# Performance work log

Hardware: AMD Instinct MI355X
Metric: run time of the kernel (lower is better)

The kernel has to match this reference:

```python
import jax, jax.numpy as jnp
import numpy as np

B, S, E, D, A, V, EM, T = 128, 196, 2048, 512, 256, 10000, 512, 20


def setup_inputs() -> dict:
    key = jax.random.key(0)
    ks = jax.random.split(key, 16)
    def rn(k, shape, scale=0.02):
        return jax.random.normal(k, shape, dtype=jnp.float32) * scale
    return {
        "encoder_features": jax.random.normal(ks[0], (B, S, E), dtype=jnp.float32),
        "captions": jax.random.randint(ks[1], (B, T), 0, V),
        "emb_table": rn(ks[2], (V, EM)),
        "W_ea": rn(ks[3], (E, A)), "b_ea": jnp.zeros((A,), jnp.float32),
        "W_da": rn(ks[4], (D, A)), "b_da": jnp.zeros((A,), jnp.float32),
        "W_fa": rn(ks[5], (A, 1)), "b_fa": jnp.zeros((1,), jnp.float32),
        "W_ih": rn(ks[6], (EM + E, 4 * D)), "b_ih": jnp.zeros((4 * D,), jnp.float32),
        "W_hh": rn(ks[7], (D, 4 * D)), "b_hh": jnp.zeros((4 * D,), jnp.float32),
        "W_cp": rn(ks[8], (E, EM)), "b_cp": jnp.zeros((EM,), jnp.float32),
        "W_hp": rn(ks[9], (D, EM)), "b_hp": jnp.zeros((EM,), jnp.float32),
        "W_op": rn(ks[10], (EM, V)), "b_op": jnp.zeros((V,), jnp.float32),
        "W_inith": rn(ks[11], (E, D)), "b_inith": jnp.zeros((D,), jnp.float32),
        "W_initc": rn(ks[12], (E, D)), "b_initc": jnp.zeros((D,), jnp.float32),
    }


def reference(encoder_features, captions, emb_table, W_ea, b_ea, W_da, b_da,
              W_fa, b_fa, W_ih, b_ih, W_hh, b_hh, W_cp, b_cp, W_hp, b_hp,
              W_op, b_op, W_inith, b_inith, W_initc, b_initc):
    # init LSTM state from mean-pooled encoder features
    mean_feat = encoder_features.mean(axis=1)            # [B, E]
    h0 = mean_feat @ W_inith + b_inith                   # [B, D]
    c0 = mean_feat @ W_initc + b_initc                   # [B, D]
    # encoder branch of Bahdanau attention is step-invariant: precompute
    enc_att = jnp.einsum('bse,ea->bsa', encoder_features, W_ea) + b_ea  # [B, S, A]
    embs = emb_table[captions]                           # [B, T, EM]
    xs = jnp.swapaxes(embs, 0, 1)                        # [T, B, EM]

    def step(carry, x_t):
        h, c = carry
        # Bahdanau: relu(enc_att + dec_att) -> score -> softmax -> context
        dec_att = h @ W_da + b_da                        # [B, A]
        combined = jax.nn.relu(enc_att + dec_att[:, None, :])  # [B, S, A]
        scores = (combined @ W_fa)[..., 0] + b_fa[0]     # [B, S]
        alpha = jax.nn.softmax(scores, axis=1)           # [B, S]
        context = jnp.einsum('bs,bse->be', alpha, encoder_features)  # [B, E]
        # LSTMCell on [embedding; context]
        x_in = jnp.concatenate([x_t, context], axis=-1)  # [B, EM+E]
        gates = x_in @ W_ih + b_ih + h @ W_hh + b_hh     # [B, 4D]
        i, f, g, o = jnp.split(gates, 4, axis=-1)
        c_new = jax.nn.sigmoid(f) * c + jax.nn.sigmoid(i) * jnp.tanh(g)
        h_new = jax.nn.sigmoid(o) * jnp.tanh(c_new)
        # output: proj(context) + proj(hidden) -> vocab logits (dropout = eval identity)
        feat = context @ W_cp + b_cp + h_new @ W_hp + b_hp  # [B, EM]
        logits = feat @ W_op + b_op                      # [B, V]
        return (h_new, c_new), logits

    _, logits = jax.lax.scan(step, (h0, c0), xs)         # [T, B, V]
    return jnp.swapaxes(logits, 0, 1)                    # [B, T, V]
```

## Files before the change

### kernel.cpp

```cpp
#include <hip/hip_runtime.h>
#include <hip/hip_bf16.h>

#define B 128
#define S 196
#define E 2048
#define D 512
#define A 256
#define V 10000
#define EM 512
#define T 20
#define KCAT 2560

typedef unsigned short u16;
typedef __bf16 bf16x8 __attribute__((ext_vector_type(8)));
typedef float f32x4 __attribute__((ext_vector_type(4)));
typedef u16 u16x8 __attribute__((ext_vector_type(8)));
typedef u16 u16x4 __attribute__((ext_vector_type(4)));

__device__ inline u16 f2bf(float f) {
    union { float f; unsigned u; } x; x.f = f;
    return (u16)((x.u + 0x7FFFu + ((x.u >> 16) & 1u)) >> 16);
}
__device__ inline float bf2f(u16 h) {
    union { unsigned u; float f; } x; x.u = ((unsigned)h) << 16;
    return x.f;
}
__device__ inline bf16x8 ld_bf8(const u16* p) {
    return __builtin_bit_cast(bf16x8, *reinterpret_cast<const u16x8*>(p));
}
__device__ inline bf16x8 cvt_bf8(const float* p) {
    float4 u = *reinterpret_cast<const float4*>(p);
    float4 v = *reinterpret_cast<const float4*>(p + 4);
    u16x8 t;
    t[0] = f2bf(u.x); t[1] = f2bf(u.y); t[2] = f2bf(u.z); t[3] = f2bf(u.w);
    t[4] = f2bf(v.x); t[5] = f2bf(v.y); t[6] = f2bf(v.z); t[7] = f2bf(v.w);
    return __builtin_bit_cast(bf16x8, t);
}
__device__ inline float sigm(float x) { return 1.f / (1.f + expf(-x)); }

struct PairT {
    const void* Ap;
    long lda;
    const u16* Bt;
    long ldb;
    int K;
};

template <int NP, bool AF32, typename OutT, int WTM, int WTN, int WVM, int WVN>
__global__ __launch_bounds__(WVM * WVN * 64) void gemm_mfma(
    int N, PairT q0, PairT q1, PairT q2,
    const float* __restrict__ bias1, const float* __restrict__ bias2,
    OutT* __restrict__ Cc, long ldc)
{
    const int tid  = threadIdx.x;
    const int w    = tid >> 6;
    const int lane = tid & 63;
    const int lr   = lane & 15;
    const int lg   = lane >> 4;
    const int mrow = blockIdx.y * (WVM * WTM * 16) + (w / WVN) * (WTM * 16);
    const int ncol = blockIdx.x * (WVN * WTN * 16) + (w % WVN) * (WTN * 16);

    f32x4 acc[WTM][WTN];
#pragma unroll
    for (int i = 0; i < WTM; ++i)
#pragma unroll
        for (int j = 0; j < WTN; ++j) acc[i][j] = (f32x4){0.f, 0.f, 0.f, 0.f};

    const PairT qs[3] = {q0, q1, q2};
#pragma unroll
    for (int p = 0; p < NP; ++p) {
        const PairT pp = qs[p];
        const int nk = pp.K >> 5;
        const u16*   Ab = (const u16*)pp.Ap;
        const float* Af = (const float*)pp.Ap;
        size_t aoff[WTM];
#pragma unroll
        for (int mi = 0; mi < WTM; ++mi)
            aoff[mi] = (size_t)(mrow + mi * 16 + lr) * pp.lda + lg * 8;
        const u16* Bp = pp.Bt + (size_t)(ncol + lr) * pp.ldb + lg * 8;

#pragma unroll 2
        for (int kk = 0; kk < nk; ++kk) {
            const int ko = kk * 32;
            bf16x8 av[WTM], bv[WTN];
#pragma unroll
            for (int mi = 0; mi < WTM; ++mi) {
                if (AF32) av[mi] = cvt_bf8(Af + aoff[mi] + ko);
                else      av[mi] = ld_bf8(Ab + aoff[mi] + ko);
            }
#pragma unroll
            for (int ni = 0; ni < WTN; ++ni)
                bv[ni] = ld_bf8(Bp + ko + (size_t)(ni * 16) * pp.ldb);
#pragma unroll
            for (int mi = 0; mi < WTM; ++mi)
#pragma unroll
                for (int ni = 0; ni < WTN; ++ni)
                    acc[mi][ni] = __builtin_amdgcn_mfma_f32_16x16x32_bf16(
                        av[mi], bv[ni], acc[mi][ni], 0, 0, 0);
        }
    }

#pragma unroll
    for (int ni = 0; ni < WTN; ++ni) {
        const int col = ncol + ni * 16 + lr;
        if (col >= N) continue;
        float bs = 0.f;
        if (bias1) bs += bias1[col];
        if (bias2) bs += bias2[col];
#pragma unroll
        for (int mi = 0; mi < WTM; ++mi) {
#pragma unroll
            for (int r = 0; r < 4; ++r) {
                const int row = mrow + mi * 16 + lg * 4 + r;
                const float v = acc[mi][ni][r] + bs;
                if constexpr (sizeof(OutT) == 2)
                    Cc[(size_t)row * ldc + col] = (OutT)f2bf(v);
                else
                    Cc[(size_t)row * ldc + col] = v;
            }
        }
    }
}

__global__ __launch_bounds__(256) void gemm_enc(
    const u16* __restrict__ Abf,
    const u16* __restrict__ Bt,
    const float* __restrict__ bias,
    u16* __restrict__ Cc)
{
    __shared__ u16 As[128 * 64];
    __shared__ u16 Bs[128 * 64];

    const int tid  = threadIdx.x;
    const int w    = tid >> 6;
    const int lane = tid & 63;
    const int lr   = lane & 15;
    const int lg   = lane >> 4;
    const int brow = blockIdx.y * 128;
    const int bcol = blockIdx.x * 128;
    const int wrow = (w >> 1) * 64;
    const int wcol = (w & 1) * 64;

    int arow[4], acb[4], aphys[4];
#pragma unroll
    for (int i = 0; i < 4; ++i) {
        const int s = (tid + 256 * i) * 16;
        arow[i]  = s >> 7;
        acb[i]   = s & 127;
        aphys[i] = (s ^ ((arow[i] & 7) << 4)) >> 1;
    }

    int aoff[2][4], boff[2][4];
#pragma unroll
    for (int kh = 0; kh < 2; ++kh) {
#pragma unroll
        for (int i = 0; i < 4; ++i) {
            const int ra = wrow + i * 16 + lr;
            aoff[kh][i] = (((ra << 7) + (kh << 6) + (lg << 4)) ^ ((ra & 7) << 4)) >> 1;
            const int rb = wcol + i * 16 + lr;
            boff[kh][i] = (((rb << 7) + (kh << 6) + (lg << 4)) ^ ((rb & 7) << 4)) >> 1;
        }
    }

    f32x4 acc[4][4];
#pragma unroll
    for (int i = 0; i < 4; ++i)
#pragma unroll
        for (int j = 0; j < 4; ++j) acc[i][j] = (f32x4){0.f, 0.f, 0.f, 0.f};

    for (int k0 = 0; k0 < 2048; k0 += 64) {
        u16x8 av[4], bv[4];
#pragma unroll
        for (int i = 0; i < 4; ++i) {
            av[i] = *reinterpret_cast<const u16x8*>(
                Abf + (size_t)(brow + arow[i]) * 2048 + k0 + (acb[i] >> 1));
            bv[i] = *reinterpret_cast<const u16x8*>(
                Bt + (size_t)(bcol + arow[i]) * 2048 + k0 + (acb[i] >> 1));
        }
        __syncthreads();
#pragma unroll
        for (int i = 0; i < 4; ++i) {
            *reinterpret_cast<u16x8*>(As + aphys[i]) = av[i];
            *reinterpret_cast<u16x8*>(Bs + aphys[i]) = bv[i];
        }
        __syncthreads();

#pragma unroll
        for (int kh = 0; kh < 2; ++kh) {
            bf16x8 af[4], bf_[4];
#pragma unroll
            for (int mi = 0; mi < 4; ++mi)
                af[mi] = __builtin_bit_cast(bf16x8,
                    *reinterpret_cast<const u16x8*>(As + aoff[kh][mi]));
#pragma unroll
            for (int ni = 0; ni < 4; ++ni)
                bf_[ni] = __builtin_bit_cast(bf16x8,
                    *reinterpret_cast<const u16x8*>(Bs + boff[kh][ni]));
#pragma unroll
            for (int mi = 0; mi < 4; ++mi)
#pragma unroll
                for (int ni = 0; ni < 4; ++ni)
                    acc[mi][ni] = __builtin_amdgcn_mfma_f32_16x16x32_bf16(
                        af[mi], bf_[ni], acc[mi][ni], 0, 0, 0);
        }
    }

#pragma unroll
    for (int ni = 0; ni < 4; ++ni) {
        const int col = bcol + wcol + ni * 16 + lr;
        const float bs = bias[col];
#pragma unroll
        for (int mi = 0; mi < 4; ++mi) {
#pragma unroll
            for (int r = 0; r < 4; ++r) {
                const int row = brow + wrow + mi * 16 + lg * 4 + r;
                Cc[(size_t)row * 256 + col] = f2bf(acc[mi][ni][r] + bs);
            }
        }
    }
}

__global__ __launch_bounds__(256) void init_xin_h(
    const u16* __restrict__ h_cur, u16* __restrict__ xin)
{
    const int idx = blockIdx.x * 256 + threadIdx.x;
    const int b = idx >> 9;
    const int d = idx & (D - 1);
    xin[(size_t)b * KCAT + 2048 + d] = h_cur[idx];
}

template <bool FBF>
__global__ __launch_bounds__(256) void alpha_ctx_lstm(
    const void* __restrict__ Fv,
    const u16*  __restrict__ enc,
    const u16*  __restrict__ W_daT,
    const float* __restrict__ b_da,
    const float* __restrict__ W_fa,
    const float* __restrict__ b_ih_,
    const float* __restrict__ b_hh_,
    const float* __restrict__ egates,
    const float* __restrict__ part,
    const float* __restrict__ c_rd,
    float* __restrict__ c_wr,
    const u16*  __restrict__ h0,
    u16* __restrict__ h_all,
    u16* __restrict__ ctx_all,
    u16* __restrict__ xin,
    int t)
{
    const int blk  = blockIdx.x;
    const int tid  = threadIdx.x;
    const int w    = tid >> 6;
    const int lane = tid & 63;
    const int b    = blk >> 1;
    const int q    = blk & 1;

    __shared__ float hl[D];
    __shared__ float dec[A];
    __shared__ float wfa[A];
    __shared__ float sc[S];
    __shared__ float red[8];

    if (t == 0) {
        hl[tid]       = bf2f(h0[b * D + tid]);
        hl[tid + 256] = bf2f(h0[b * D + 256 + tid]);
    } else {
        const int tt = t - 1;
#pragma unroll
        for (int half = 0; half < 2; ++half) {
            const int d = tid + half * 256;
            float g4[4];
#pragma unroll
            for (int g = 0; g < 4; ++g) {
                const int col = ((d >> 4) << 6) + (g << 4) + (d & 15);
                float s = b_ih_[g * D + d] + b_hh_[g * D + d] +
                          egates[((size_t)(b * T + tt) << 11) + col];
#pragma unroll
                for (int z = 0; z < 8; ++z)
                    s += part[((size_t)(z * B + b) << 11) + col];
                g4[g] = s;
            }
            const int idx = (b << 9) + d;
            const float cn = sigm(g4[1]) * c_rd[idx] + sigm(g4[0]) * tanhf(g4[2]);
            const float hf = sigm(g4[3]) * tanhf(cn);
            hl[d] = hf;
            if (q == 0) {
                c_wr[idx] = cn;
                const u16 hv = f2bf(hf);
                h_all[((size_t)(b * T + tt)) * D + d] = hv;
                xin[(size_t)b * KCAT + 2048 + d] = hv;
            }
        }
    }
    wfa[tid] = W_fa[tid];
    __syncthreads();

    {
        float acc = 0.f;
        const u16* wr = W_daT + (size_t)tid * D;
#pragma unroll 4
        for (int i = 0; i < D / 8; ++i) {
            const u16x8 v = *reinterpret_cast<const u16x8*>(wr + i * 8);
#pragma unroll
            for (int j = 0; j < 8; ++j) acc += bf2f(v[j]) * hl[i * 8 + j];
        }
        dec[tid] = acc + b_da[tid];
    }
    __syncthreads();

    if (tid < S) {
        const u16* er = enc + ((size_t)b * S + tid) * A;
        float v = 0.f;
#pragma unroll 4
        for (int i = 0; i < A / 8; ++i) {
            const u16x8 e8 = *reinterpret_cast<const u16x8*>(er + i * 8);
#pragma unroll
            for (int j = 0; j < 8; ++j) {
                float x = bf2f(e8[j]) + dec[i * 8 + j];
                x = x > 0.f ? x : 0.f;
                v += x * wfa[i * 8 + j];
            }
        }
        sc[tid] = v;
    }
    __syncthreads();

    float m = -1e30f;
    for (int s = tid; s < S; s += 256) m = fmaxf(m, sc[s]);
    for (int off = 32; off; off >>= 1) m = fmaxf(m, __shfl_down(m, off));
    if (lane == 0) red[w] = m;
    __syncthreads();
    if (tid == 0) red[0] = fmaxf(fmaxf(red[0], red[1]), fmaxf(red[2], red[3]));
    __syncthreads();
    m = red[0];

    float sum = 0.f;
    for (int s = tid; s < S; s += 256) {
        const float ev = __expf(sc[s] - m);
        sc[s] = ev;
        sum += ev;
    }
    for (int off = 32; off; off >>= 1) sum += __shfl_down(sum, off);
    if (lane == 0) red[4 + w] = sum;
    __syncthreads();
    if (tid == 0) red[4] = red[4] + red[5] + red[6] + red[7];
    __syncthreads();
    const float inv = 1.f / red[4];

    {
        const int e0 = q * 1024 + tid * 4;
        float a0 = 0.f, a1 = 0.f, a2 = 0.f, a3 = 0.f;
        float b0 = 0.f, b1 = 0.f, b2 = 0.f, b3 = 0.f;
        float c0 = 0.f, c1 = 0.f, c2 = 0.f, c3 = 0.f;
        float d0 = 0.f, d1 = 0.f, d2 = 0.f, d3 = 0.f;
        if (FBF) {
            const u16* F0 = (const u16*)Fv + (size_t)b * S * E + e0;
            const u16* F1 = F0 + (size_t)49 * E;
            const u16* F2 = F0 + (size_t)98 * E;
            const u16* F3 = F0 + (size_t)147 * E;
#pragma unroll 7
            for (int s = 0; s < 49; ++s) {
                const u16x4 v0 = *reinterpret_cast<const u16x4*>(F0 + (size_t)s * E);
                const u16x4 v1 = *reinterpret_cast<const u16x4*>(F1 + (size_t)s * E);
                const u16x4 v2 = *reinterpret_cast<const u16x4*>(F2 + (size_t)s * E);
                const u16x4 v3 = *reinterpret_cast<const u16x4*>(F3 + (size_t)s * E);
                const float l0 = sc[s], l1 = sc[s + 49], l2 = sc[s + 98], l3 = sc[s + 147];
                a0 += l0 * bf2f(v0[0]); a1 += l0 * bf2f(v0[1]);
                a2 += l0 * bf2f(v0[2]); a3 += l0 * bf2f(v0[3]);
                b0 += l1 * bf2f(v1[0]); b1 += l1 * bf2f(v1[1]);
                b2 += l1 * bf2f(v1[2]); b3 += l1 * bf2f(v1[3]);
                c0 += l2 * bf2f(v2[0]); c1 += l2 * bf2f(v2[1]);
                c2 += l2 * bf2f(v2[2]); c3 += l2 * bf2f(v2[3]);
                d0 += l3 * bf2f(v3[0]); d1 += l3 * bf2f(v3[1]);
                d2 += l3 * bf2f(v3[2]); d3 += l3 * bf2f(v3[3]);
            }
        } else {
            const float* F0 = (const float*)Fv + (size_t)b * S * E + e0;
            const float* F1 = F0 + (size_t)49 * E;
            const float* F2 = F0 + (size_t)98 * E;
            const float* F3 = F0 + (size_t)147 * E;
#pragma unroll 7
            for (int s = 0; s < 49; ++s) {
                const float4 v0 = *reinterpret_cast<const float4*>(F0 + (size_t)s * E);
                const float4 v1 = *reinterpret_cast<const float4*>(F1 + (size_t)s * E);
                const float4 v2 = *reinterpret_cast<const float4*>(F2 + (size_t)s * E);
                const float4 v3 = *reinterpret_cast<const float4*>(F3 + (size_t)s * E);
                const float l0 = sc[s], l1 = sc[s + 49], l2 = sc[s + 98], l3 = sc[s + 147];
                a0 += l0 * v0.x; a1 += l0 * v0.y; a2 += l0 * v0.z; a3 += l0 * v0.w;
                b0 += l1 * v1.x; b1 += l1 * v1.y; b2 += l1 * v1.z; b3 += l1 * v1.w;
                c0 += l2 * v2.x; c1 += l2 * v2.y; c2 += l2 * v2.z; c3 += l2 * v2.w;
                d0 += l3 * v3.x; d1 += l3 * v3.y; d2 += l3 * v3.z; d3 += l3 * v3.w;
            }
        }
        a0 += b0 + c0 + d0; a1 += b1 + c1 + d1;
        a2 += b2 + c2 + d2; a3 += b3 + c3 + d3;
        u16x4 o;
        o[0] = f2bf(a0 * inv); o[1] = f2bf(a1 * inv);
        o[2] = f2bf(a2 * inv); o[3] = f2bf(a3 * inv);
        *reinterpret_cast<u16x4*>(ctx_all + ((size_t)(b * T + t)) * E + e0) = o;
        *reinterpret_cast<u16x4*>(xin + (size_t)b * KCAT + e0) = o;
    }
}

__global__ __launch_bounds__(128) void gates_split8(
    const u16* __restrict__ xin, const u16* __restrict__ W_chT,
    float* __restrict__ part)
{
    const int tid  = threadIdx.x;
    const int w    = tid >> 6;
    const int lane = tid & 63;
    const int lr   = lane & 15;
    const int lg   = lane >> 4;
    const int mrow = blockIdx.y * 16;
    const int ncol = blockIdx.x * 128 + w * 64;
    const int z    = blockIdx.z;
    const int kb   = z * 320;

    f32x4 acc[4];
#pragma unroll
    for (int j = 0; j < 4; ++j) acc[j] = (f32x4){0.f, 0.f, 0.f, 0.f};

    const u16* Ap = xin + (size_t)(mrow + lr) * KCAT + kb + lg * 8;
    const u16* Bp = W_chT + (size_t)(ncol + lr) * KCAT + kb + lg * 8;

#pragma unroll
    for (int kk = 0; kk < 10; ++kk) {
        const int ko = kk * 32;
        const bf16x8 av = ld_bf8(Ap + ko);
        bf16x8 bv[4];
#pragma unroll
        for (int ni = 0; ni < 4; ++ni)
            bv[ni] = ld_bf8(Bp + ko + (size_t)(ni * 16) * KCAT);
#pragma unroll
        for (int ni = 0; ni < 4; ++ni)
            acc[ni] = __builtin_amdgcn_mfma_f32_16x16x32_bf16(av, bv[ni], acc[ni], 0, 0, 0);
    }

#pragma unroll
    for (int ni = 0; ni < 4; ++ni) {
        const int col = ncol + ni * 16 + lr;
#pragma unroll
        for (int r = 0; r < 4; ++r) {
            const int row = mrow + lg * 4 + r;
            part[((size_t)(z * B + row) << 11) + col] = acc[ni][r];
        }
    }
}

__global__ __launch_bounds__(256) void lstm_last(
    const float* __restrict__ part,
    const float* __restrict__ egates,
    const float* __restrict__ b_ih_, const float* __restrict__ b_hh_,
    const float* __restrict__ c_rd,
    u16* __restrict__ h_all)
{
    const int idx = blockIdx.x * 256 + threadIdx.x;
    const int b = idx >> 9;
    const int d = idx & (D - 1);
    const int tt = T - 1;
    float g4[4];
#pragma unroll
    for (int g = 0; g < 4; ++g) {
        const int col = ((d >> 4) << 6) + (g << 4) + (d & 15);
        float s = b_ih_[g * D + d] + b_hh_[g * D + d] +
                  egates[((size_t)(b * T + tt) << 11) + col];
#pragma unroll
        for (int z = 0; z < 8; ++z)
            s += part[((size_t)(z * B + b) << 11) + col];
        g4[g] = s;
    }
    const float cn = sigm(g4[1]) * c_rd[idx] + sigm(g4[0]) * tanhf(g4[2]);
    h_all[((size_t)(b * T + tt)) * D + d] = f2bf(sigm(g4[3]) * tanhf(cn));
}

__global__ __launch_bounds__(256) void transpose_bf(
    const float* __restrict__ in, int K, int N, u16* __restrict__ out)
{
    __shared__ float tls[32][33];
    const int k0 = blockIdx.y * 32, n0 = blockIdx.x * 32;
    const int c = threadIdx.x & 31, r8 = threadIdx.x >> 5;
#pragma unroll
    for (int i = 0; i < 4; ++i) {
        const int k = r8 + i * 8;
        float v = 0.f;
        if (n0 + c < N) v = in[(size_t)(k0 + k) * N + n0 + c];
        tls[k][c] = v;
    }
    __syncthreads();
#pragma unroll
    for (int i = 0; i < 4; ++i) {
        const int n = r8 + i * 8;
        out[(size_t)(n0 + n) * K + k0 + c] = f2bf(tls[c][n]);
    }
}

__global__ __launch_bounds__(256) void transpose_bf_gates(
    const float* __restrict__ in, int Kin, u16* __restrict__ out, int ldo, int ko)
{
    __shared__ float tls[32][33];
    const int k0 = blockIdx.y * 32, n0 = blockIdx.x * 32;
    const int c = threadIdx.x & 31, r8 = threadIdx.x >> 5;
#pragma unroll
    for (int i = 0; i < 4; ++i) {
        const int k = r8 + i * 8;
        tls[k][c] = in[(size_t)(k0 + k) * 2048 + n0 + c];
    }
    __syncthreads();
#pragma unroll
    for (int i = 0; i < 4; ++i) {
        const int nn = r8 + i * 8;
        const int n = n0 + nn;
        const int g = n >> 9, d = n & (D - 1);
        const int orow = ((d >> 4) << 6) + (g << 4) + (d & 15);
        out[(size_t)orow * ldo + ko + k0 + c] = f2bf(tls[c][nn]);
    }
}

template <bool WRITE>
__global__ __launch_bounds__(256) void conv_mean(
    const float* __restrict__ F, u16* __restrict__ Fbf, u16* __restrict__ meanbf)
{
    const int idx = blockIdx.x * 256 + threadIdx.x;
    const int b = idx >> 11;
    const int e = idx & (E - 1);
    const float* src = F + (size_t)b * S * E + e;
    float acc = 0.f;
#pragma unroll 2
    for (int s = 0; s < S; ++s) {
        const float v = src[(size_t)s * E];
        acc += v;
        if (WRITE) Fbf[(size_t)b * S * E + (size_t)s * E + e] = f2bf(v);
    }
    meanbf[idx] = f2bf(acc * (1.f / (float)S));
}

__global__ __launch_bounds__(256) void gather_embs_bf(
    const int* __restrict__ captions, const float* __restrict__ table,
    u16* __restrict__ out)
{
    const int idx = blockIdx.x * 256 + threadIdx.x;
    const int row = idx >> 6;
    const int ch  = idx & 63;
    const int cap = captions[row];
    const float* src = table + (size_t)cap * EM + ch * 8;
    float4 u = *reinterpret_cast<const float4*>(src);
    float4 v = *reinterpret_cast<const float4*>(src + 4);
    u16x8 t;
    t[0] = f2bf(u.x); t[1] = f2bf(u.y); t[2] = f2bf(u.z); t[3] = f2bf(u.w);
    t[4] = f2bf(v.x); t[5] = f2bf(v.y); t[6] = f2bf(v.z); t[7] = f2bf(v.w);
    *reinterpret_cast<u16x8*>(out + (size_t)row * EM + ch * 8) = t;
}

struct Pair {
    const float* Aptr; int lda; const float* Wptr; int ldw; int K;
};

template <int NP>
__global__ __launch_bounds__(256) void gemm_f32(
    int M, int N, Pair p0, Pair p1, Pair p2,
    const float* __restrict__ bias1, const float* __restrict__ bias2,
    float* __restrict__ C, long ldc)
{
    __shared__ float As[64][17];
    __shared__ float Ws[16][64];
    const int tid = threadIdx.x;
    const int row0 = blockIdx.y * 64, col0 = blockIdx.x * 64;
    const int tx = tid & 15, ty = tid >> 4;
    float acc[4][4] = {};
    Pair ps[3] = {p0, p1, p2};
#pragma unroll
    for (int p = 0; p < NP; ++p) {
        const float* Ag = ps[p].Aptr; const float* Wg = ps[p].Wptr;
        const int lda = ps[p].lda, ldw = ps[p].ldw, K = ps[p].K;
        for (int k0 = 0; k0 < K; k0 += 16) {
            {
                const int k = tid & 15, mb = tid >> 4;
#pragma unroll
                for (int i = 0; i < 4; ++i) {
                    const int m = mb + 16 * i, gr = row0 + m;
                    float v = 0.f;
                    if (gr < M) v = Ag[(size_t)gr * lda + k0 + k];
                    As[m][k] = v;
                }
            }
            {
                const int n = tid & 63, kb = tid >> 6, gc = col0 + n;
#pragma unroll
                for (int i = 0; i < 4; ++i) {
                    const int k = kb * 4 + i;
                    float v = 0.f;
                    if (gc < N) v = Wg[(size_t)(k0 + k) * ldw + gc];
                    Ws[k][n] = v;
                }
            }
            __syncthreads();
#pragma unroll
            for (int k = 0; k < 16; ++k) {
                float av[4];
#pragma unroll
                for (int i = 0; i < 4; ++i) av[i] = As[ty * 4 + i][k];
                const float4 bv = reinterpret_cast<const float4*>(&Ws[k][0])[tx];
                const float bvv[4] = {bv.x, bv.y, bv.z, bv.w};
#pragma unroll
                for (int i = 0; i < 4; ++i)
#pragma unroll
                    for (int j = 0; j < 4; ++j) acc[i][j] += av[i] * bvv[j];
            }
            __syncthreads();
        }
    }
#pragma unroll
    for (int i = 0; i < 4; ++i) {
        const int r = row0 + ty * 4 + i;
        if (r >= M) continue;
#pragma unroll
        for (int j = 0; j < 4; ++j) {
            const int cidx = col0 + tx * 4 + j;
            if (cidx >= N) continue;
            float v = acc[i][j];
            if (bias1) v += bias1[cidx];
            if (bias2) v += bias2[cidx];
            C[(size_t)r * ldc + cidx] = v;
        }
    }
}

__global__ __launch_bounds__(256) void mean_pool(const float* __restrict__ F,
                                                 float* __restrict__ mean)
{
    const int idx = blockIdx.x * 256 + threadIdx.x;
    const int b = idx >> 11, e = idx & (E - 1);
    const float* Fb = F + (size_t)b * S * E + e;
    float acc = 0.f;
    for (int s = 0; s < S; ++s) acc += Fb[(size_t)s * E];
    mean[idx] = acc * (1.f / (float)S);
}

__global__ __launch_bounds__(256) void gather_embs(const int* __restrict__ captions,
                                                   const float* __restrict__ table,
                                                   float* __restrict__ out)
{
    const int idx = blockIdx.x * 256 + threadIdx.x;
    const int per_row = EM / 4;
    const int row = idx / per_row;
    const int col = idx - row * per_row;
    const int cap = captions[row];
    reinterpret_cast<float4*>(out)[idx] =
        reinterpret_cast<const float4*>(table + (size_t)cap * EM)[col];
}

__global__ __launch_bounds__(256) void attn_softmax(
    const float* __restrict__ enc_att, const float* __restrict__ dec_att,
    const float* __restrict__ W_fa, const float* __restrict__ b_fa,
    float* __restrict__ alpha)
{
    const int b = blockIdx.x, tid = threadIdx.x;
    const int wave = tid >> 6, lane = tid & 63;
    __shared__ float dec[A], wfa[A], sc[S], redm[4], reds[4];
    dec[tid] = dec_att[b * A + tid];
    wfa[tid] = W_fa[tid];
    __syncthreads();
    for (int s = wave; s < S; s += 4) {
        const float* ea = enc_att + ((size_t)b * S + s) * A;
        float v = 0.f;
#pragma unroll
        for (int i = 0; i < 4; ++i) {
            const int a = lane + 64 * i;
            float x = ea[a] + dec[a];
            x = x > 0.f ? x : 0.f;
            v += x * wfa[a];
        }
        for (int off = 32; off; off >>= 1) v += __shfl_down(v, off);
        if (lane == 0) sc[s] = v + b_fa[0];
    }
    __syncthreads();
    float m = -1e30f;
    for (int s = tid; s < S; s += 256) m = fmaxf(m, sc[s]);
    for (int off = 32; off; off >>= 1) m = fmaxf(m, __shfl_down(m, off));
    if (lane == 0) redm[wave] = m;
    __syncthreads();
    if (tid == 0) redm[0] = fmaxf(fmaxf(redm[0], redm[1]), fmaxf(redm[2], redm[3]));
    __syncthreads();
    m = redm[0];
    float sum = 0.f;
    for (int s = tid; s < S; s += 256) {
        const float ev = expf(sc[s] - m);
        sc[s] = ev; sum += ev;
    }
    for (int off = 32; off; off >>= 1) sum += __shfl_down(sum, off);
    if (lane == 0) reds[wave] = sum;
    __syncthreads();
    if (tid == 0) reds[0] = reds[0] + reds[1] + reds[2] + reds[3];
    __syncthreads();
    const float inv = 1.f / reds[0];
    for (int s = tid; s < S; s += 256) alpha[b * S + s] = sc[s] * inv;
}

__global__ __launch_bounds__(256) void context_kernel(
    const float* __restrict__ F, const float* __restrict__ alpha,
    float* __restrict__ ctx)
{
    const int chunks = E / 256;
    const int b = blockIdx.x / chunks;
    const int ec = blockIdx.x - b * chunks;
    const int e = ec * 256 + threadIdx.x;
    __shared__ float al[S];
    for (int s = threadIdx.x; s < S; s += 256) al[s] = alpha[b * S + s];
    __syncthreads();
    const float* Fb = F + (size_t)b * S * E + e;
    float acc = 0.f;
    for (int s = 0; s < S; ++s) acc += al[s] * Fb[(size_t)s * E];
    ctx[b * E + e] = acc;
}

__global__ __launch_bounds__(256) void lstm_cell(
    const float* __restrict__ gates, float* __restrict__ h, float* __restrict__ c)
{
    const int idx = blockIdx.x * 256 + threadIdx.x;
    const int b = idx >> 9, d = idx & (D - 1);
    const float* g = gates + (size_t)b * 4 * D;
    const float gi = g[d], gf = g[D + d], gg = g[2 * D + d], go = g[3 * D + d];
    const float cn = sigm(gf) * c[idx] + sigm(gi) * tanhf(gg);
    c[idx] = cn;
    h[idx] = sigm(go) * tanhf(cn);
}

extern "C" void kernel_launch(void* const* d_in, const int* in_sizes, int n_in,
                              void* d_out, int out_size, void* d_ws, size_t ws_size,
                              hipStream_t stream)
{
    const float* F        = (const float*)d_in[0];
    const int*   captions = (const int*)  d_in[1];
    const float* table    = (const float*)d_in[2];
    const float* W_ea     = (const float*)d_in[3];
    const float* b_ea     = (const float*)d_in[4];
    const float* W_da     = (const float*)d_in[5];
    const float* b_da     = (const float*)d_in[6];
    const float* W_fa     = (const float*)d_in[7];
    const float* b_fa     = (const float*)d_in[8];
    const float* W_ih     = (const float*)d_in[9];
    const float* b_ih     = (const float*)d_in[10];
    const float* W_hh     = (const float*)d_in[11];
    const float* b_hh     = (const float*)d_in[12];
    const float* W_cp     = (const float*)d_in[13];
    const float* b_cp     = (const float*)d_in[14];
    const float* W_hp     = (const float*)d_in[15];
    const float* b_hp     = (const float*)d_in[16];
    const float* W_op     = (const float*)d_in[17];
    const float* b_op     = (const float*)d_in[18];
    const float* W_inith  = (const float*)d_in[19];
    const float* b_inith  = (const float*)d_in[20];
    const float* W_initc  = (const float*)d_in[21];
    const float* b_initc  = (const float*)d_in[22];

    float* out = (float*)d_out;
    const int VP2 = 10240;

    char* base = (char*)d_ws;
    size_t off = 0;
    auto alloc = [&](size_t bytes) -> void* {
        off = (off + 255) & ~(size_t)255;
        void* p = base + off;
        off += bytes;
        return p;
    };

    u16* W_eaT    = (u16*)alloc((size_t)A * E * 2);
    u16* W_daT    = (u16*)alloc((size_t)A * D * 2);
    u16* W_iheT   = (u16*)alloc((size_t)2048 * EM * 2);
    u16* W_chT    = (u16*)alloc((size_t)2048 * KCAT * 2);
    u16* W_cpT    = (u16*)alloc((size_t)EM * E * 2);
    u16* W_hpT    = (u16*)alloc((size_t)EM * D * 2);
    u16* W_opT    = (u16*)alloc((size_t)VP2 * EM * 2);
    u16* W_inithT = (u16*)alloc((size_t)D * E * 2);
    u16* W_initcT = (u16*)alloc((size_t)D * E * 2);
    u16* embs     = (u16*)alloc((size_t)B * T * EM * 2);
    u16* mean_bf  = (u16*)alloc((size_t)B * E * 2);
    u16* h_cur    = (u16*)alloc((size_t)B * D * 2);
    u16* h_all    = (u16*)alloc((size_t)B * T * D * 2);
    u16* ctx_all  = (u16*)alloc((size_t)B * T * E * 2);
    u16* xin      = (u16*)alloc((size_t)B * KCAT * 2);
    u16* feat_all = (u16*)alloc((size_t)B * T * EM * 2);
    u16* enc_bf   = (u16*)alloc((size_t)B * S * A * 2);
    float* cbuf0  = (float*)alloc((size_t)B * D * 4);
    float* cbuf1  = (float*)alloc((size_t)B * D * 4);
    float* egates = (float*)alloc((size_t)B * T * 2048 * 4);
    float* part   = (float*)alloc((size_t)8 * B * 2048 * 4);
    const size_t need_base = off;
    u16* F_bf     = (u16*)alloc((size_t)B * S * E * 2);
    const size_t need_fbf = off;

    const bool ok_base = need_base <= ws_size;
    const bool ok_fbf  = need_fbf <= ws_size;

    if (!ok_base) {
        float* ws = (float*)d_ws;
        float* mean_feat = ws;  ws += B * E;
        float* h         = ws;  ws += B * D;
        float* c         = ws;  ws += B * D;
        float* enc_att   = ws;  ws += (size_t)B * S * A;
        float* fembs     = ws;  ws += (size_t)B * T * EM;
        float* fdec      = ws;  ws += B * A;
        float* falpha    = ws;  ws += B * S;
        float* fctx      = ws;  ws += B * E;
        float* fgates    = ws;  ws += B * 4 * D;
        float* ffeat     = ws;  ws += B * EM;
        const Pair ZP = {nullptr, 0, nullptr, 0, 0};
        mean_pool<<<(B * E) / 256, 256, 0, stream>>>(F, mean_feat);
        { Pair p = {mean_feat, E, W_inith, D, E};
          gemm_f32<1><<<dim3(D / 64, B / 64), 256, 0, stream>>>(B, D, p, ZP, ZP, b_inith, nullptr, h, D); }
        { Pair p = {mean_feat, E, W_initc, D, E};
          gemm_f32<1><<<dim3(D / 64, B / 64), 256, 0, stream>>>(B, D, p, ZP, ZP, b_initc, nullptr, c, D); }
        { Pair p = {F, E, W_ea, A, E};
          gemm_f32<1><<<dim3(A / 64, (B * S) / 64), 256, 0, stream>>>(B * S, A, p, ZP, ZP, b_ea, nullptr, enc_att, A); }
        gather_embs<<<(B * T * (EM / 4)) / 256, 256, 0, stream>>>(captions, table, fembs);
        for (int t = 0; t < T; ++t) {
            { Pair p = {h, D, W_da, A, D};
              gemm_f32<1><<<dim3(A / 64, B / 64), 256, 0, stream>>>(B, A, p, ZP, ZP, b_da, nullptr, fdec, A); }
            attn_softmax<<<B, 256, 0, stream>>>(enc_att, fdec, W_fa, b_fa, falpha);
            context_kernel<<<B * (E / 256), 256, 0, stream>>>(F, falpha, fctx);
            { Pair p0 = {fembs + (size_t)t * EM, T * EM, W_ih, 4 * D, EM};
              Pair p1 = {fctx, E, W_ih + (size_t)EM * 4 * D, 4 * D, E};
              Pair p2 = {h, D, W_hh, 4 * D, D};
              gemm_f32<3><<<dim3((4 * D) / 64, B / 64), 256, 0, stream>>>(B, 4 * D, p0, p1, p2, b_ih, b_hh, fgates, 4 * D); }
            lstm_cell<<<(B * D) / 256, 256, 0, stream>>>(fgates, h, c);
            { Pair p0 = {fctx, E, W_cp, EM, E};
              Pair p1 = {h, D, W_hp, EM, D};
              gemm_f32<2><<<dim3(EM / 64, B / 64), 256, 0, stream>>>(B, EM, p0, p1, ZP, b_cp, b_hp, ffeat, EM); }
            { Pair p = {ffeat, EM, W_op, V, EM};
              gemm_f32<1><<<dim3((V + 63) / 64, B / 64), 256, 0, stream>>>(B, V, p, ZP, ZP, b_op, nullptr, out + (size_t)t * V, (long)T * V); }
        }
        return;
    }

    const PairT ZP = {nullptr, 0, nullptr, 0, 0};

    transpose_bf<<<dim3(A / 32, E / 32), 256, 0, stream>>>(W_ea, E, A, W_eaT);
    transpose_bf<<<dim3(A / 32, D / 32), 256, 0, stream>>>(W_da, D, A, W_daT);
    transpose_bf_gates<<<dim3(64, EM / 32), 256, 0, stream>>>(W_ih, EM, W_iheT, EM, 0);
    transpose_bf_gates<<<dim3(64, E / 32), 256, 0, stream>>>(W_ih + (size_t)EM * 2048, E, W_chT, KCAT, 0);
    transpose_bf_gates<<<dim3(64, D / 32), 256, 0, stream>>>(W_hh, D, W_chT, KCAT, 2048);
    transpose_bf<<<dim3(EM / 32, E / 32), 256, 0, stream>>>(W_cp, E, EM, W_cpT);
    transpose_bf<<<dim3(EM / 32, D / 32), 256, 0, stream>>>(W_hp, D, EM, W_hpT);
    transpose_bf<<<dim3(VP2 / 32, EM / 32), 256, 0, stream>>>(W_op, EM, V, W_opT);
    transpose_bf<<<dim3(D / 32, E / 32), 256, 0, stream>>>(W_inith, E, D, W_inithT);
    transpose_bf<<<dim3(D / 32, E / 32), 256, 0, stream>>>(W_initc, E, D, W_initcT);

    if (ok_fbf)
        conv_mean<true><<<(B * E) / 256, 256, 0, stream>>>(F, F_bf, mean_bf);
    else
        conv_mean<false><<<(B * E) / 256, 256, 0, stream>>>(F, nullptr, mean_bf);

    gather_embs_bf<<<(B * T * (EM / 8)) / 256, 256, 0, stream>>>(captions, table, embs);

    { PairT p = {mean_bf, E, W_inithT, E, E};
      gemm_mfma<1, false, u16, 2, 4, 1, 4><<<dim3(2, 4), 256, 0, stream>>>(
          D, p, ZP, ZP, b_inith, nullptr, h_cur, D); }
    { PairT p = {mean_bf, E, W_initcT, E, E};
      gemm_mfma<1, false, float, 2, 4, 1, 4><<<dim3(2, 4), 256, 0, stream>>>(
          D, p, ZP, ZP, b_initc, nullptr, cbuf1, D); }

    init_xin_h<<<(B * D) / 256, 256, 0, stream>>>(h_cur, xin);

    if (ok_fbf) {
        gemm_enc<<<dim3(2, (B * S) / 128), 256, 0, stream>>>(F_bf, W_eaT, b_ea, enc_bf);
    } else {
        PairT p = {F, E, W_eaT, E, E};
        gemm_mfma<1, true, u16, 4, 4, 1, 4><<<dim3(1, (B * S) / 64), 256, 0, stream>>>(
            A, p, ZP, ZP, b_ea, nullptr, enc_bf, A);
    }

    { PairT p = {embs, EM, W_iheT, EM, EM};
      gemm_mfma<1, false, float, 2, 4, 2, 2><<<dim3(16, 40), 256, 0, stream>>>(
          2048, p, ZP, ZP, nullptr, nullptr, egates, 2048); }

    for (int t = 0; t < T; ++t) {
        const int tt = t - 1;
        const float* crd = (tt >= 0 && (tt & 1)) ? cbuf0 : cbuf1;
        float*       cwr = (tt >= 0 && (tt & 1)) ? cbuf1 : cbuf0;

        if (ok_fbf)
            alpha_ctx_lstm<true><<<256, 256, 0, stream>>>(
                F_bf, enc_bf, W_daT, b_da, W_fa, b_ih, b_hh, egates, part,
                crd, cwr, h_cur, h_all, ctx_all, xin, t);
        else
            alpha_ctx_lstm<false><<<256, 256, 0, stream>>>(
                F, enc_bf, W_daT, b_da, W_fa, b_ih, b_hh, egates, part,
                crd, cwr, h_cur, h_all, ctx_all, xin, t);

        gates_split8<<<dim3(16, 8, 8), 128, 0, stream>>>(xin, W_chT, part);
    }

    lstm_last<<<(B * D) / 256, 256, 0, stream>>>(
        part, egates, b_ih, b_hh, ((T - 1) & 1) ? cbuf0 : cbuf1, h_all);

    { PairT p0 = {ctx_all, E, W_cpT, E, E};
      PairT p1 = {h_all, D, W_hpT, D, D};
      gemm_mfma<2, false, u16, 1, 4, 2, 2><<<dim3(EM / 128, (B * T) / 32), 256, 0, stream>>>(
          EM, p0, p1, ZP, b_cp, b_hp, feat_all, EM); }

    { PairT p = {feat_all, EM, W_opT, EM, EM};
      gemm_mfma<1, false, float, 4, 4, 2, 2><<<dim3(VP2 / 128, (B * T) / 128), 256, 0, stream>>>(
          V, p, ZP, ZP, b_op, nullptr, out, V); }
}
```

Before: 1.543 ms.

## Merge weight transposes into one launch, halve gates K-split, swap GEMM grid order

The ten separate weight-transpose launches become a single transpose_all kernel that finds its segment from a flattened block index, cutting launch overhead. The per-step recurrent gates GEMM now splits K four ways instead of eight, so it writes and later reduces half as many partial sums, at the cost of half as many blocks per step. Several GEMM launches swap the grid x/y mapping so consecutive blocks walk along M and reuse the same weight columns, which should improve cache locality.

```diff
diff --git a/kernel.cpp b/kernel.cpp
--- a/kernel.cpp
+++ b/kernel.cpp
@@ -46,7 +46,8 @@
     int K;
 };
 
-template <int NP, bool AF32, typename OutT, int WTM, int WTN, int WVM, int WVN>
+template <int NP, bool AF32, typename OutT, int WTM, int WTN, int WVM, int WVN,
+          bool SWAPXY = false>
 __global__ __launch_bounds__(WVM * WVN * 64) void gemm_mfma(
     int N, PairT q0, PairT q1, PairT q2,
     const float* __restrict__ bias1, const float* __restrict__ bias2,
@@ -57,8 +58,10 @@
     const int lane = tid & 63;
     const int lr   = lane & 15;
     const int lg   = lane >> 4;
-    const int mrow = blockIdx.y * (WVM * WTM * 16) + (w / WVN) * (WTM * 16);
-    const int ncol = blockIdx.x * (WVN * WTN * 16) + (w % WVN) * (WTN * 16);
+    const int mb   = SWAPXY ? blockIdx.x : blockIdx.y;
+    const int nb   = SWAPXY ? blockIdx.y : blockIdx.x;
+    const int mrow = mb * (WVM * WTM * 16) + (w / WVN) * (WTM * 16);
+    const int ncol = nb * (WVN * WTN * 16) + (w % WVN) * (WTN * 16);
 
     f32x4 acc[WTM][WTN];
 #pragma unroll
@@ -276,7 +279,7 @@
                 float s = b_ih_[g * D + d] + b_hh_[g * D + d] +
                           egates[((size_t)(b * T + tt) << 11) + col];
 #pragma unroll
-                for (int z = 0; z < 8; ++z)
+                for (int z = 0; z < 4; ++z)
                     s += part[((size_t)(z * B + b) << 11) + col];
                 g4[g] = s;
             }
@@ -402,7 +405,7 @@
     }
 }
 
-__global__ __launch_bounds__(128) void gates_split8(
+__global__ __launch_bounds__(128) void gates_split4(
     const u16* __restrict__ xin, const u16* __restrict__ W_chT,
     float* __restrict__ part)
 {
@@ -414,7 +417,7 @@
     const int mrow = blockIdx.y * 16;
     const int ncol = blockIdx.x * 128 + w * 64;
     const int z    = blockIdx.z;
-    const int kb   = z * 320;
+    const int kb   = z * 640;
 
     f32x4 acc[4];
 #pragma unroll
@@ -423,8 +426,8 @@
     const u16* Ap = xin + (size_t)(mrow + lr) * KCAT + kb + lg * 8;
     const u16* Bp = W_chT + (size_t)(ncol + lr) * KCAT + kb + lg * 8;
 
-#pragma unroll
-    for (int kk = 0; kk < 10; ++kk) {
+#pragma unroll 4
+    for (int kk = 0; kk < 20; ++kk) {
         const int ko = kk * 32;
         const bf16x8 av = ld_bf8(Ap + ko);
         bf16x8 bv[4];
@@ -465,7 +468,7 @@
         float s = b_ih_[g * D + d] + b_hh_[g * D + d] +
                   egates[((size_t)(b * T + tt) << 11) + col];
 #pragma unroll
-        for (int z = 0; z < 8; ++z)
+        for (int z = 0; z < 4; ++z)
             s += part[((size_t)(z * B + b) << 11) + col];
         g4[g] = s;
     }
@@ -473,46 +476,44 @@
     h_all[((size_t)(b * T + tt)) * D + d] = f2bf(sigm(g4[3]) * tanhf(cn));
 }
 
-__global__ __launch_bounds__(256) void transpose_bf(
-    const float* __restrict__ in, int K, int N, u16* __restrict__ out)
+struct TSeg {
+    const float* src; u16* dst;
+    int K; int N; int ldo; int ko; int mode; int tilesX; int nblk;
+};
+struct TransArgs { TSeg seg[10]; };
+
+__global__ __launch_bounds__(256) void transpose_all(TransArgs a)
 {
     __shared__ float tls[32][33];
-    const int k0 = blockIdx.y * 32, n0 = blockIdx.x * 32;
-    const int c = threadIdx.x & 31, r8 = threadIdx.x >> 5;
+    int bid = blockIdx.x;
+    int si = 0;
+    while (si < 9 && bid >= a.seg[si].nblk) { bid -= a.seg[si].nblk; ++si; }
+    const TSeg s = a.seg[si];
+    const int n0 = (bid % s.tilesX) * 32;
+    const int k0 = (bid / s.tilesX) * 32;
+    const int c  = threadIdx.x & 31;
+    const int r8 = threadIdx.x >> 5;
+
 #pragma unroll
     for (int i = 0; i < 4; ++i) {
         const int k = r8 + i * 8;
         float v = 0.f;
-        if (n0 + c < N) v = in[(size_t)(k0 + k) * N + n0 + c];
+        if (n0 + c < s.N) v = s.src[(size_t)(k0 + k) * s.N + n0 + c];
         tls[k][c] = v;
-    }
-    __syncthreads();
-#pragma unroll
-    for (int i = 0; i < 4; ++i) {
-        const int n = r8 + i * 8;
-        out[(size_t)(n0 + n) * K + k0 + c] = f2bf(tls[c][n]);
-    }
-}
-
-__global__ __launch_bounds__(256) void transpose_bf_gates(
-    const float* __restrict__ in, int Kin, u16* __restrict__ out, int ldo, int ko)
-{
-    __shared__ float tls[32][33];
-    const int k0 = blockIdx.y * 32, n0 = blockIdx.x * 32;
-    const int c = threadIdx.x & 31, r8 = threadIdx.x >> 5;
-#pragma unroll
-    for (int i = 0; i < 4; ++i) {
-        const int k = r8 + i * 8;
-        tls[k][c] = in[(size_t)(k0 + k) * 2048 + n0 + c];
     }
     __syncthreads();
 #pragma unroll
     for (int i = 0; i < 4; ++i) {
         const int nn = r8 + i * 8;
         const int n = n0 + nn;
-        const int g = n >> 9, d = n & (D - 1);
-        const int orow = ((d >> 4) << 6) + (g << 4) + (d & 15);
-        out[(size_t)orow * ldo + ko + k0 + c] = f2bf(tls[c][nn]);
+        int row;
+        if (s.mode) {
+            const int g = n >> 9, d = n & (D - 1);
+            row = ((d >> 4) << 6) + (g << 4) + (d & 15);
+        } else {
+            row = n;
+        }
+        s.dst[(size_t)row * s.ldo + s.ko + k0 + c] = f2bf(tls[c][nn]);
     }
 }
 
@@ -785,7 +786,7 @@
     float* cbuf0  = (float*)alloc((size_t)B * D * 4);
     float* cbuf1  = (float*)alloc((size_t)B * D * 4);
     float* egates = (float*)alloc((size_t)B * T * 2048 * 4);
-    float* part   = (float*)alloc((size_t)8 * B * 2048 * 4);
+    float* part   = (float*)alloc((size_t)4 * B * 2048 * 4);
     const size_t need_base = off;
     u16* F_bf     = (u16*)alloc((size_t)B * S * E * 2);
     const size_t need_fbf = off;
@@ -835,16 +836,26 @@
 
     const PairT ZP = {nullptr, 0, nullptr, 0, 0};
 
-    transpose_bf<<<dim3(A / 32, E / 32), 256, 0, stream>>>(W_ea, E, A, W_eaT);
-    transpose_bf<<<dim3(A / 32, D / 32), 256, 0, stream>>>(W_da, D, A, W_daT);
-    transpose_bf_gates<<<dim3(64, EM / 32), 256, 0, stream>>>(W_ih, EM, W_iheT, EM, 0);
-    transpose_bf_gates<<<dim3(64, E / 32), 256, 0, stream>>>(W_ih + (size_t)EM * 2048, E, W_chT, KCAT, 0);
-    transpose_bf_gates<<<dim3(64, D / 32), 256, 0, stream>>>(W_hh, D, W_chT, KCAT, 2048);
-    transpose_bf<<<dim3(EM / 32, E / 32), 256, 0, stream>>>(W_cp, E, EM, W_cpT);
-    transpose_bf<<<dim3(EM / 32, D / 32), 256, 0, stream>>>(W_hp, D, EM, W_hpT);
-    transpose_bf<<<dim3(VP2 / 32, EM / 32), 256, 0, stream>>>(W_op, EM, V, W_opT);
-    transpose_bf<<<dim3(D / 32, E / 32), 256, 0, stream>>>(W_inith, E, D, W_inithT);
-    transpose_bf<<<dim3(D / 32, E / 32), 256, 0, stream>>>(W_initc, E, D, W_initcT);
+    {
+        TransArgs ta;
+        auto seg = [&](int i, const float* src, u16* dst, int K, int N,
+                       int ldo, int ko, int mode, int tilesX) {
+            ta.seg[i] = {src, dst, K, N, ldo, ko, mode, tilesX, tilesX * (K / 32)};
+        };
+        seg(0, W_ea,    W_eaT,    2048, 256,   2048, 0,    0, 8);
+        seg(1, W_da,    W_daT,    512,  256,   512,  0,    0, 8);
+        seg(2, W_ih,    W_iheT,   512,  2048,  512,  0,    1, 64);
+        seg(3, W_ih + (size_t)EM * 2048, W_chT, 2048, 2048, KCAT, 0, 1, 64);
+        seg(4, W_hh,    W_chT,    512,  2048,  KCAT, 2048, 1, 64);
+        seg(5, W_cp,    W_cpT,    2048, 512,   2048, 0,    0, 16);
+        seg(6, W_hp,    W_hpT,    512,  512,   512,  0,    0, 16);
+        seg(7, W_op,    W_opT,    512,  10000, 512,  0,    0, 320);
+        seg(8, W_inith, W_inithT, 2048, 512,   2048, 0,    0, 16);
+        seg(9, W_initc, W_initcT, 2048, 512,   2048, 0,    0, 16);
+        int tot = 0;
+        for (int i = 0; i < 10; ++i) tot += ta.seg[i].nblk;
+        transpose_all<<<tot, 256, 0, stream>>>(ta);
+    }
 
     if (ok_fbf)
         conv_mean<true><<<(B * E) / 256, 256, 0, stream>>>(F, F_bf, mean_bf);
@@ -871,7 +882,7 @@
     }
 
     { PairT p = {embs, EM, W_iheT, EM, EM};
-      gemm_mfma<1, false, float, 2, 4, 2, 2><<<dim3(16, 40), 256, 0, stream>>>(
+      gemm_mfma<1, false, float, 2, 4, 2, 2, true><<<dim3(40, 16), 256, 0, stream>>>(
           2048, p, ZP, ZP, nullptr, nullptr, egates, 2048); }
 
     for (int t = 0; t < T; ++t) {
@@ -888,7 +899,7 @@
                 F, enc_bf, W_daT, b_da, W_fa, b_ih, b_hh, egates, part,
                 crd, cwr, h_cur, h_all, ctx_all, xin, t);
 
-        gates_split8<<<dim3(16, 8, 8), 128, 0, stream>>>(xin, W_chT, part);
+        gates_split4<<<dim3(16, 8, 4), 128, 0, stream>>>(xin, W_chT, part);
     }
 
     lstm_last<<<(B * D) / 256, 256, 0, stream>>>(
@@ -896,10 +907,10 @@
 
     { PairT p0 = {ctx_all, E, W_cpT, E, E};
       PairT p1 = {h_all, D, W_hpT, D, D};
-      gemm_mfma<2, false, u16, 1, 4, 2, 2><<<dim3(EM / 128, (B * T) / 32), 256, 0, stream>>>(
+      gemm_mfma<2, false, u16, 1, 4, 2, 2, true><<<dim3((B * T) / 32, EM / 128), 256, 0, stream>>>(
           EM, p0, p1, ZP, b_cp, b_hp, feat_all, EM); }
 
     { PairT p = {feat_all, EM, W_opT, EM, EM};
-      gemm_mfma<1, false, float, 4, 4, 2, 2><<<dim3(VP2 / 128, (B * T) / 128), 256, 0, stream>>>(
+      gemm_mfma<1, false, float, 4, 4, 2, 2, true><<<dim3((B * T) / 128, VP2 / 128), 256, 0, stream>>>(
           V, p, ZP, ZP, b_op, nullptr, out, V); }
 }
```

New measurement: 1.513 ms. Within noise of the previous version (-1.9%).
